# Kernel tuning notes

Measured on AMD Instinct MI355X. Metric: run time of the kernel, lower is better.

The kernel has to match this reference:

```python
import jax, jax.numpy as jnp
import numpy as np

NUM_HEADS = 16
HEAD_DIM = 64


def setup_inputs() -> dict:
    key = jax.random.key(0)
    k1, k2, k3 = jax.random.split(key, 3)
    B, S, D = 2, 2048, 1024
    scale = 1.0 / np.sqrt(D)
    return {
        "x": jax.random.normal(k1, (B, S, D), dtype=jnp.float32),
        "W_qkv": jax.random.normal(k2, (D, 3 * D), dtype=jnp.float32) * scale,
        "b_qkv": jnp.zeros((3 * D,), dtype=jnp.float32),
        "W_o": jax.random.normal(k3, (D, D), dtype=jnp.float32) * scale,
        "b_o": jnp.zeros((D,), dtype=jnp.float32),
    }


def reference(x, W_qkv, b_qkv, W_o, b_o):
    B, S, D = x.shape
    H, Hd = NUM_HEADS, HEAD_DIM
    qkv = x @ W_qkv + b_qkv                      # [B, S, 3D]
    qkv = qkv.reshape(B, S, H, 3 * Hd).transpose(0, 2, 1, 3)  # [B, H, S, 3Hd]
    q, k, v = jnp.split(qkv, 3, axis=-1)         # each [B, H, S, Hd]
    # negative squared Euclidean distance: -(|q|^2 - 2 q.k + |k|^2)
    q_sq = jnp.sum(q * q, axis=-1)[..., :, None]   # [B, H, S, 1]
    k_sq = jnp.sum(k * k, axis=-1)[..., None, :]   # [B, H, 1, S]
    qk = jnp.einsum("bhsd,bhtd->bhst", q, k)       # [B, H, S, S]
    logits = -(q_sq - 2.0 * qk + k_sq)
    attn = jax.nn.softmax(logits, axis=-1)
    vals = jnp.einsum("bhst,bhtd->bhsd", attn, v)  # [B, H, S, Hd]
    vals = vals.transpose(0, 2, 1, 3).reshape(B, S, D)
    return vals @ W_o + b_o
```

## Files before the change

kernel.cpp:

```cpp
#include <hip/hip_runtime.h>
#include <hip/hip_bf16.h>

#define NUM_B   2
#define SEQ     2048
#define DMODEL  1024
#define NH      16
#define HD      64
#define M_TOT   (NUM_B * SEQ)
#define N_QKV   (3 * DMODEL)
#define LOG2E   1.4426950408889634f
#define EXP_BIAS 96.0f

typedef __attribute__((ext_vector_type(8))) short short8v;
typedef __attribute__((ext_vector_type(4))) float float4v;
typedef unsigned short ushort_t;

__device__ __forceinline__ ushort_t f2bf(float x) {
    unsigned u = __builtin_bit_cast(unsigned, x);
    u = u + 0x7FFFu + ((u >> 16) & 1u);
    return (ushort_t)(u >> 16);
}
__device__ __forceinline__ float bf2f(ushort_t h) {
    unsigned u = ((unsigned)h) << 16;
    return __builtin_bit_cast(float, u);
}
__device__ __forceinline__ void gll16(const void* g, void* l) {
    __builtin_amdgcn_global_load_lds(
        (const __attribute__((address_space(1))) unsigned int*)g,
        (__attribute__((address_space(3))) unsigned int*)l, 16, 0, 0);
}
__device__ __forceinline__ int sw4(int r) { return (r & 3) ^ ((r >> 2) & 3); }

__global__ __launch_bounds__(256) void prep_kernel(
    const float* __restrict__ Wq, const float* __restrict__ Wo,
    const float* __restrict__ Xf,
    ushort_t* __restrict__ WqT_hi, ushort_t* __restrict__ WqT_lo,
    ushort_t* __restrict__ WoT,
    ushort_t* __restrict__ Xhi, ushort_t* __restrict__ Xlo)
{
    const int bid = blockIdx.x;
    const int t = threadIdx.x;

    if (bid >= 1024) {
        size_t base = (size_t)(bid - 1024) * 4096 + t * 16;
        float xs[16];
        *(float4v*)&xs[0]  = *(const float4v*)(Xf + base);
        *(float4v*)&xs[4]  = *(const float4v*)(Xf + base + 4);
        *(float4v*)&xs[8]  = *(const float4v*)(Xf + base + 8);
        *(float4v*)&xs[12] = *(const float4v*)(Xf + base + 12);
        short8v h0, h1, l0, l1;
        #pragma unroll
        for (int e = 0; e < 8; e++) {
            ushort_t a = f2bf(xs[e]), b = f2bf(xs[8 + e]);
            h0[e] = (short)a; h1[e] = (short)b;
            l0[e] = (short)f2bf(xs[e] - bf2f(a));
            l1[e] = (short)f2bf(xs[8 + e] - bf2f(b));
        }
        *(short8v*)(Xhi + base) = h0; *(short8v*)(Xhi + base + 8) = h1;
        *(short8v*)(Xlo + base) = l0; *(short8v*)(Xlo + base + 8) = l1;
        return;
    }

    __shared__ float Tf[64][65];
    const float* src; ushort_t *dhi, *dlo; int N, k0, n0;
    if (bid < 768) {
        int kt = bid / 48, nt = bid % 48;
        src = Wq; N = N_QKV; dhi = WqT_hi; dlo = WqT_lo;
        k0 = kt * 64; n0 = nt * 64;
    } else {
        int tid = bid - 768;
        int kt = tid >> 4, nt = tid & 15;
        src = Wo; N = DMODEL; dhi = WoT; dlo = nullptr;
        k0 = kt * 64; n0 = nt * 64;
    }
    {
        int r = t >> 2, c0 = (t & 3) * 16;
        const float* srow = src + (size_t)(k0 + r) * N + n0 + c0;
        #pragma unroll
        for (int u = 0; u < 4; u++) {
            float4v f = *(const float4v*)(srow + 4 * u);
            #pragma unroll
            for (int e = 0; e < 4; e++) Tf[r][c0 + 4 * u + e] = f[e];
        }
    }
    __syncthreads();
    {
        int nl = t >> 2, kc = (t & 3) * 16;
        short8v h0, h1, l0, l1;
        #pragma unroll
        for (int e = 0; e < 8; e++) {
            float x0 = Tf[kc + e][nl];
            float x1 = Tf[kc + 8 + e][nl];
            ushort_t a = f2bf(x0), b = f2bf(x1);
            h0[e] = (short)a; h1[e] = (short)b;
            l0[e] = (short)f2bf(x0 - bf2f(a));
            l1[e] = (short)f2bf(x1 - bf2f(b));
        }
        ushort_t* o = dhi + (size_t)(n0 + nl) * 1024 + k0 + kc;
        *(short8v*)o = h0; *(short8v*)(o + 8) = h1;
        if (dlo) {
            ushort_t* o2 = dlo + (size_t)(n0 + nl) * 1024 + k0 + kc;
            *(short8v*)o2 = l0; *(short8v*)(o2 + 8) = l1;
        }
    }
}

template<bool PRE>
__global__ __launch_bounds__(256) void qkv_mfma_kernel(
    const float* __restrict__ X,
    const ushort_t* __restrict__ Xhi, const ushort_t* __restrict__ Xlo,
    const ushort_t* __restrict__ WqT_hi, const ushort_t* __restrict__ WqT_lo,
    const float* __restrict__ bias,
    ushort_t* __restrict__ Qhi, ushort_t* __restrict__ Qlo,
    ushort_t* __restrict__ Khi, ushort_t* __restrict__ Klo,
    ushort_t* __restrict__ Vout,
    float* __restrict__ Qsq, float* __restrict__ Ksq)
{
    __shared__ ushort_t AS2[2 * 128 * 32];
    __shared__ ushort_t BS [2 * 128 * 32];
    const int LO = 128 * 32;
    const int t = threadIdx.x;
    const int w = t >> 6, lane = t & 63;
    const int quad = (t >> 4) & 3, ln = t & 15;
    const int wr = w >> 1, wc = w & 1;
    const int m0 = blockIdx.y * 128, n0 = blockIdx.x * 128;
    const int g = blockIdx.x * 2 + wc;
    const int h = g / 3, part = g % 3;

    const ushort_t* gA[2]; ushort_t* lA[2];
    const float* aptr = nullptr;
    ushort_t *ast_hi0, *ast_hi1, *ast_lo0, *ast_lo1;
    size_t xlo_off = 0;
    if constexpr (PRE) {
        #pragma unroll
        for (int i = 0; i < 2; i++) {
            int c = 256 * i + 64 * w + lane;
            int r = c >> 2, kbp = c & 3;
            gA[i] = Xhi + (size_t)(m0 + r) * 1024 + 8 * (kbp ^ sw4(r));
            lA[i] = &AS2[(256 * i + 64 * w) * 8];
        }
        xlo_off = (size_t)(Xlo - Xhi);
    } else {
        const int arow = t >> 1, akh = t & 1;
        aptr = X + (size_t)(m0 + arow) * DMODEL + 16 * akh;
        const int asw = sw4(arow);
        ast_hi0 = &AS2[arow * 32 + (((2 * akh) ^ asw) << 3)];
        ast_hi1 = &AS2[arow * 32 + (((2 * akh + 1) ^ asw) << 3)];
        ast_lo0 = &AS2[LO + arow * 32 + (((2 * akh) ^ asw) << 3)];
        ast_lo1 = &AS2[LO + arow * 32 + (((2 * akh + 1) ^ asw) << 3)];
    }

    const ushort_t* gB[2]; ushort_t* lB[2];
    #pragma unroll
    for (int i = 0; i < 2; i++) {
        int c = 256 * i + 64 * w + lane;
        int n = c >> 2, kbp = c & 3;
        gB[i] = WqT_hi + (size_t)(n0 + n) * 1024 + 8 * (kbp ^ sw4(n));
        lB[i] = &BS[(256 * i + 64 * w) * 8];
    }
    const size_t lo_goff = (size_t)(WqT_lo - WqT_hi);

    int aoff[4], boff[4];
    #pragma unroll
    for (int i = 0; i < 4; i++) {
        int m_l = 64 * wr + 16 * i + ln;
        aoff[i] = m_l * 32 + ((quad ^ sw4(m_l)) << 3);
        int n_l = 64 * wc + 16 * i + ln;
        boff[i] = n_l * 32 + ((quad ^ sw4(n_l)) << 3);
    }

    float4v acc[4][4];
    #pragma unroll
    for (int i = 0; i < 4; i++)
        #pragma unroll
        for (int j = 0; j < 4; j++) acc[i][j] = (float4v){0.f, 0.f, 0.f, 0.f};

    for (int k0 = 0; k0 < DMODEL; k0 += 32) {
        __syncthreads();
        #pragma unroll
        for (int i = 0; i < 2; i++) {
            gll16(gB[i] + k0, lB[i]);
            gll16(gB[i] + k0 + lo_goff, lB[i] + LO);
        }
        if constexpr (PRE) {
            #pragma unroll
            for (int i = 0; i < 2; i++) {
                gll16(gA[i] + k0, lA[i]);
                gll16(gA[i] + k0 + xlo_off, lA[i] + LO);
            }
        } else {
            float xs[16];
            *(float4v*)&xs[0]  = *(const float4v*)(aptr + k0);
            *(float4v*)&xs[4]  = *(const float4v*)(aptr + k0 + 4);
            *(float4v*)&xs[8]  = *(const float4v*)(aptr + k0 + 8);
            *(float4v*)&xs[12] = *(const float4v*)(aptr + k0 + 12);
            short8v h0, h1, l0, l1;
            #pragma unroll
            for (int e = 0; e < 8; e++) {
                ushort_t a = f2bf(xs[e]), b = f2bf(xs[8 + e]);
                h0[e] = (short)a; h1[e] = (short)b;
                l0[e] = (short)f2bf(xs[e] - bf2f(a));
                l1[e] = (short)f2bf(xs[8 + e] - bf2f(b));
            }
            *(short8v*)ast_hi0 = h0; *(short8v*)ast_hi1 = h1;
            *(short8v*)ast_lo0 = l0; *(short8v*)ast_lo1 = l1;
        }
        __syncthreads();

        short8v ah[4], al[4], bh[4], bl[4];
        #pragma unroll
        for (int i = 0; i < 4; i++) {
            ah[i] = *(short8v*)&AS2[aoff[i]];
            al[i] = *(short8v*)&AS2[LO + aoff[i]];
            bh[i] = *(short8v*)&BS[boff[i]];
            bl[i] = *(short8v*)&BS[LO + boff[i]];
        }
        if (part != 2) {
            #pragma unroll
            for (int mt = 0; mt < 4; mt++)
                #pragma unroll
                for (int nt = 0; nt < 4; nt++) {
                    acc[mt][nt] = __builtin_amdgcn_mfma_f32_16x16x32_bf16(ah[mt], bh[nt], acc[mt][nt], 0, 0, 0);
                    acc[mt][nt] = __builtin_amdgcn_mfma_f32_16x16x32_bf16(ah[mt], bl[nt], acc[mt][nt], 0, 0, 0);
                    acc[mt][nt] = __builtin_amdgcn_mfma_f32_16x16x32_bf16(al[mt], bh[nt], acc[mt][nt], 0, 0, 0);
                }
        } else {
            #pragma unroll
            for (int mt = 0; mt < 4; mt++)
                #pragma unroll
                for (int nt = 0; nt < 4; nt++)
                    acc[mt][nt] = __builtin_amdgcn_mfma_f32_16x16x32_bf16(ah[mt], bh[nt], acc[mt][nt], 0, 0, 0);
        }
    }

    float bvv[4];
    #pragma unroll
    for (int nt = 0; nt < 4; nt++) bvv[nt] = bias[64 * g + 16 * nt + ln];

    #pragma unroll
    for (int mt = 0; mt < 4; mt++) {
        #pragma unroll
        for (int r = 0; r < 4; r++) {
            int m = m0 + 64 * wr + 16 * mt + 4 * quad + r;
            int bb = m >> 11, s = m & (SEQ - 1);
            size_t hsrow = (size_t)(bb * NH + h) * SEQ + s;
            size_t rowbase = hsrow * HD;
            float vv[4];
            #pragma unroll
            for (int nt = 0; nt < 4; nt++) vv[nt] = acc[mt][nt][r] + bvv[nt];
            if (part == 0) {
                float sq = 0.f;
                #pragma unroll
                for (int nt = 0; nt < 4; nt++) {
                    float v = vv[nt];
                    sq += v * v;
                    float v2 = v * (2.0f * LOG2E);
                    ushort_t hb = f2bf(v2);
                    Qhi[rowbase + 16 * nt + ln] = hb;
                    Qlo[rowbase + 16 * nt + ln] = f2bf(v2 - bf2f(hb));
                }
                sq += __shfl_xor(sq, 1); sq += __shfl_xor(sq, 2);
                sq += __shfl_xor(sq, 4); sq += __shfl_xor(sq, 8);
                if (ln == 0) Qsq[hsrow] = sq * LOG2E - EXP_BIAS;
            } else if (part == 1) {
                float sq = 0.f;
                #pragma unroll
                for (int nt = 0; nt < 4; nt++) {
                    float v = vv[nt];
                    sq += v * v;
                    ushort_t hb = f2bf(v);
                    Khi[rowbase + 16 * nt + ln] = hb;
                    Klo[rowbase + 16 * nt + ln] = f2bf(v - bf2f(hb));
                }
                sq += __shfl_xor(sq, 1); sq += __shfl_xor(sq, 2);
                sq += __shfl_xor(sq, 4); sq += __shfl_xor(sq, 8);
                if (ln == 0) Ksq[hsrow] = sq * LOG2E;
            } else {
                if constexpr (PRE) {
                    #pragma unroll
                    for (int nt = 0; nt < 4; nt++)
                        Vout[((size_t)(bb * NH + h) * 64 + 16 * nt + ln) * SEQ + s] = f2bf(vv[nt]);
                } else {
                    #pragma unroll
                    for (int nt = 0; nt < 4; nt++)
                        Vout[rowbase + 16 * nt + ln] = f2bf(vv[nt]);
                }
            }
        }
    }
}

template<bool PRE>
__global__ __launch_bounds__(256, 4) void attn_mfma_kernel(
    const ushort_t* __restrict__ Qhi, const ushort_t* __restrict__ Qlo,
    const ushort_t* __restrict__ Khi, const ushort_t* __restrict__ Klo,
    const ushort_t* __restrict__ Vsrc,
    const float* __restrict__ Qsq, const float* __restrict__ Ksq,
    ushort_t* __restrict__ vals)
{
    __shared__ ushort_t KS[2 * 64 * 64];
    __shared__ ushort_t VtS [64 * 64];
    __shared__ ushort_t PsS [64 * 72];
    const int LO = 64 * 64;

    const int t    = threadIdx.x;
    const int w    = t >> 6, lane = t & 63;
    const int quad = (t >> 4) & 3, ln = t & 15;
    const int bh   = blockIdx.y;
    const int q0   = blockIdx.x * 64;
    const size_t base  = (size_t)bh * SEQ * HD;
    const size_t baseS = (size_t)bh * SEQ;

    short8v qhi[2], qlo[2];
    float4v qsq4;
    {
        size_t ro = base + (size_t)(q0 + 16 * w + ln) * HD + quad * 8;
        qhi[0] = *(const short8v*)(Qhi + ro);
        qhi[1] = *(const short8v*)(Qhi + ro + 32);
        qlo[0] = *(const short8v*)(Qlo + ro);
        qlo[1] = *(const short8v*)(Qlo + ro + 32);
        qsq4 = *(const float4v*)(Qsq + baseS + q0 + 16 * w + 4 * quad);
    }

    const ushort_t* gK[2]; ushort_t* lK[2];
    #pragma unroll
    for (int i = 0; i < 2; i++) {
        int c = 256 * i + 64 * w + lane;
        int key = c >> 3, dbp = c & 7;
        gK[i] = Khi + base + (size_t)key * HD + 8 * (dbp ^ (key & 7));
        lK[i] = &KS[(256 * i + 64 * w) * 8];
    }
    const size_t kloff = (size_t)(Klo - Khi);

    const ushort_t* gV[2]; ushort_t* lV[2];
    if constexpr (PRE) {
        #pragma unroll
        for (int i = 0; i < 2; i++) {
            int c = 256 * i + 64 * w + lane;
            int d = c >> 3, kc = c & 7;
            gV[i] = Vsrc + ((size_t)bh * 64 + d) * SEQ + 8 * (kc ^ (d & 7));
            lV[i] = &VtS[(256 * i + 64 * w) * 8];
        }
    }

    float4v accO[4];
    float lsum[4];
    #pragma unroll
    for (int nt = 0; nt < 4; nt++) accO[nt] = (float4v){0.f, 0.f, 0.f, 0.f};
    #pragma unroll
    for (int r = 0; r < 4; r++) lsum[r] = 0.f;

    for (int kt = 0; kt < SEQ; kt += 64) {
        __syncthreads();
        #pragma unroll
        for (int i = 0; i < 2; i++) {
            gll16(gK[i] + (size_t)kt * HD, lK[i]);
            gll16(gK[i] + (size_t)kt * HD + kloff, lK[i] + LO);
        }
        if constexpr (PRE) {
            #pragma unroll
            for (int i = 0; i < 2; i++)
                gll16(gV[i] + kt, lV[i]);
        } else {
            #pragma unroll
            for (int i = 0; i < 2; i++) {
                int c = t + 256 * i;
                int key = c >> 3, db = c & 7;
                short8v v8 = *(const short8v*)(Vsrc + base + (size_t)(kt + key) * HD + 8 * db);
                #pragma unroll
                for (int e = 0; e < 8; e++) {
                    int col = key ^ (e << 3);
                    VtS[(8 * db + e) * 64 + col] = (ushort_t)v8[e];
                }
            }
        }
        float ksq_c[4];
        #pragma unroll
        for (int nt = 0; nt < 4; nt++)
            ksq_c[nt] = Ksq[baseS + kt + 16 * nt + ln];
        __syncthreads();

        float4v accS[4];
        #pragma unroll
        for (int nt = 0; nt < 4; nt++) accS[nt] = (float4v){0.f, 0.f, 0.f, 0.f};

        #pragma unroll
        for (int nt = 0; nt < 4; nt++) {
            int keyrow = 16 * nt + ln;
            #pragma unroll
            for (int c = 0; c < 2; c++) {
                int db  = quad + 4 * c;
                int off = keyrow * 64 + ((db ^ (keyrow & 7)) << 3);
                short8v bh_ = *(short8v*)&KS[off];
                short8v bl_ = *(short8v*)&KS[LO + off];
                accS[nt] = __builtin_amdgcn_mfma_f32_16x16x32_bf16(qhi[c], bh_, accS[nt], 0, 0, 0);
                accS[nt] = __builtin_amdgcn_mfma_f32_16x16x32_bf16(qhi[c], bl_, accS[nt], 0, 0, 0);
                accS[nt] = __builtin_amdgcn_mfma_f32_16x16x32_bf16(qlo[c], bh_, accS[nt], 0, 0, 0);
            }
        }

        #pragma unroll
        for (int nt = 0; nt < 4; nt++) {
            float pv[4];
            #pragma unroll
            for (int r = 0; r < 4; r++) {
                float p = exp2f(accS[nt][r] - ksq_c[nt] - qsq4[r]);
                lsum[r] += p;
                pv[r] = p;
            }
            unsigned int pk01, pk23;
            asm("v_cvt_pk_bf16_f32 %0, %1, %2" : "=v"(pk01) : "v"(pv[0]), "v"(pv[1]));
            asm("v_cvt_pk_bf16_f32 %0, %1, %2" : "=v"(pk23) : "v"(pv[2]), "v"(pv[3]));
            ushort_t* pp = &PsS[(16 * w + 4 * quad) * 72 + 16 * nt + ln];
            pp[0]       = (ushort_t)(pk01 & 0xffffu);
            pp[72]      = (ushort_t)(pk01 >> 16);
            pp[144]     = (ushort_t)(pk23 & 0xffffu);
            pp[216]     = (ushort_t)(pk23 >> 16);
        }
        __syncthreads();

        #pragma unroll
        for (int c = 0; c < 2; c++) {
            short8v aP = *(short8v*)&PsS[(16 * w + ln) * 72 + quad * 8 + 32 * c];
            #pragma unroll
            for (int nt = 0; nt < 4; nt++) {
                int drow = 16 * nt + ln;
                int db   = quad + 4 * c;
                int off  = drow * 64 + ((db ^ (drow & 7)) << 3);
                short8v bV = *(short8v*)&VtS[off];
                accO[nt] = __builtin_amdgcn_mfma_f32_16x16x32_bf16(aP, bV, accO[nt], 0, 0, 0);
            }
        }
    }

    const int bb = bh >> 4, h = bh & 15;
    float inv[4];
    #pragma unroll
    for (int r = 0; r < 4; r++) {
        float s = lsum[r];
        s += __shfl_xor(s, 1); s += __shfl_xor(s, 2);
        s += __shfl_xor(s, 4); s += __shfl_xor(s, 8);
        inv[r] = 1.f / s;
    }
    #pragma unroll
    for (int nt = 0; nt < 4; nt++)
        #pragma unroll
        for (int r = 0; r < 4; r++) {
            int row = q0 + 16 * w + 4 * quad + r;
            vals[(size_t)(bb * SEQ + row) * DMODEL + h * 64 + 16 * nt + ln] =
                f2bf(accO[nt][r] * inv[r]);
        }
}

__global__ __launch_bounds__(256) void out_mfma_kernel(
    const ushort_t* __restrict__ Ab, const ushort_t* __restrict__ BT,
    const float* __restrict__ bias, float* __restrict__ out)
{
    __shared__ ushort_t AS[128 * 32], BSo[128 * 32];
    const int t = threadIdx.x;
    const int w = t >> 6, lane = t & 63;
    const int quad = (t >> 4) & 3, ln = t & 15;
    const int wr = w >> 1, wc = w & 1;
    const int m0 = blockIdx.y * 128, n0 = blockIdx.x * 128;

    const ushort_t* gA[2]; const ushort_t* gB[2];
    ushort_t *lA[2], *lB[2];
    #pragma unroll
    for (int i = 0; i < 2; i++) {
        int c = 256 * i + 64 * w + lane;
        int r = c >> 2, kbp = c & 3;
        gA[i] = Ab + (size_t)(m0 + r) * 1024 + 8 * (kbp ^ sw4(r));
        gB[i] = BT + (size_t)(n0 + r) * 1024 + 8 * (kbp ^ sw4(r));
        lA[i] = &AS[(256 * i + 64 * w) * 8];
        lB[i] = &BSo[(256 * i + 64 * w) * 8];
    }
    int aoff[4], boff[4];
    #pragma unroll
    for (int i = 0; i < 4; i++) {
        int m_l = 64 * wr + 16 * i + ln;
        aoff[i] = m_l * 32 + ((quad ^ sw4(m_l)) << 3);
        int n_l = 64 * wc + 16 * i + ln;
        boff[i] = n_l * 32 + ((quad ^ sw4(n_l)) << 3);
    }

    float4v acc[4][4];
    #pragma unroll
    for (int i = 0; i < 4; i++)
        #pragma unroll
        for (int j = 0; j < 4; j++) acc[i][j] = (float4v){0.f, 0.f, 0.f, 0.f};

    for (int k0 = 0; k0 < DMODEL; k0 += 32) {
        __syncthreads();
        #pragma unroll
        for (int i = 0; i < 2; i++) {
            gll16(gA[i] + k0, lA[i]);
            gll16(gB[i] + k0, lB[i]);
        }
        __syncthreads();
        short8v a[4], b[4];
        #pragma unroll
        for (int i = 0; i < 4; i++) {
            a[i] = *(short8v*)&AS[aoff[i]];
            b[i] = *(short8v*)&BSo[boff[i]];
        }
        #pragma unroll
        for (int mt = 0; mt < 4; mt++)
            #pragma unroll
            for (int nt = 0; nt < 4; nt++)
                acc[mt][nt] = __builtin_amdgcn_mfma_f32_16x16x32_bf16(a[mt], b[nt], acc[mt][nt], 0, 0, 0);
    }

    #pragma unroll
    for (int nt = 0; nt < 4; nt++) {
        int n = n0 + 64 * wc + 16 * nt + ln;
        float bv = bias[n];
        #pragma unroll
        for (int mt = 0; mt < 4; mt++)
            #pragma unroll
            for (int r = 0; r < 4; r++) {
                int m = m0 + 64 * wr + 16 * mt + 4 * quad + r;
                out[(size_t)m * DMODEL + n] = acc[mt][nt][r] + bv;
            }
    }
}

extern "C" void kernel_launch(void* const* d_in, const int* in_sizes, int n_in,
                              void* d_out, int out_size, void* d_ws, size_t ws_size,
                              hipStream_t stream) {
    const float* x     = (const float*)d_in[0];
    const float* W_qkv = (const float*)d_in[1];
    const float* b_qkv = (const float*)d_in[2];
    const float* W_o   = (const float*)d_in[3];
    const float* b_o   = (const float*)d_in[4];
    float* out = (float*)d_out;

    const size_t WQT = (size_t)N_QKV * DMODEL;
    const size_t WO  = (size_t)DMODEL * DMODEL;
    const size_t QE  = (size_t)NUM_B * NH * SEQ * HD;
    const size_t SQN = (size_t)NUM_B * NH * SEQ;

    const size_t NEED = (2 * WQT + WO + 5 * QE + 2 * QE) * 2 + 2 * SQN * 4;
    const bool pre = (ws_size >= NEED);

    ushort_t* ws     = (ushort_t*)d_ws;
    ushort_t* WqT_hi = ws;
    ushort_t* WqT_lo = WqT_hi + WQT;
    ushort_t* WoT    = WqT_lo + WQT;
    ushort_t* Qhi    = WoT + WO;
    ushort_t* Qlo    = Qhi + QE;
    ushort_t* Khi    = Qlo + QE;
    ushort_t* Klo    = Khi + QE;
    ushort_t* Vx     = Klo + QE;
    float*    Qsq; float* Ksq;
    ushort_t* valsb; ushort_t* Xhi = nullptr; ushort_t* Xlo = nullptr;

    if (pre) {
        Qsq   = (float*)(Vx + QE);
        Ksq   = Qsq + SQN;
        Xhi   = (ushort_t*)(Ksq + SQN);
        Xlo   = Xhi + QE;
        valsb = WqT_hi;
    } else {
        valsb = Vx + QE;
        Qsq   = (float*)(valsb + QE);
        Ksq   = Qsq + SQN;
    }

    prep_kernel<<<pre ? 2048 : 1024, 256, 0, stream>>>(
        W_qkv, W_o, x, WqT_hi, WqT_lo, WoT, Xhi, Xlo);
    if (pre) {
        qkv_mfma_kernel<true><<<dim3(N_QKV / 128, M_TOT / 128), 256, 0, stream>>>(
            x, Xhi, Xlo, WqT_hi, WqT_lo, b_qkv, Qhi, Qlo, Khi, Klo, Vx, Qsq, Ksq);
        attn_mfma_kernel<true><<<dim3(SEQ / 64, NUM_B * NH), 256, 0, stream>>>(
            Qhi, Qlo, Khi, Klo, Vx, Qsq, Ksq, valsb);
    } else {
        qkv_mfma_kernel<false><<<dim3(N_QKV / 128, M_TOT / 128), 256, 0, stream>>>(
            x, nullptr, nullptr, WqT_hi, WqT_lo, b_qkv, Qhi, Qlo, Khi, Klo, Vx, Qsq, Ksq);
        attn_mfma_kernel<false><<<dim3(SEQ / 64, NUM_B * NH), 256, 0, stream>>>(
            Qhi, Qlo, Khi, Klo, Vx, Qsq, Ksq, valsb);
    }
    out_mfma_kernel<<<dim3(DMODEL / 128, M_TOT / 128), 256, 0, stream>>>(
        valsb, WoT, b_o, out);
}
```

Measured before the change: 311.0 us.

## Add 256x256-tile QKV GEMM kernel with part-specialized split-bf16 precision

Adds a new QKV projection kernel that uses 512 threads and a 256x256 output tile, with double-buffered LDS staging via direct global-to-LDS loads. Each block handles a single Q, K or V part across four heads. The three-term hi/lo bf16 compensation is applied only to the Q/K parts, while V uses one bf16 MFMA. This aims to raise data reuse per LDS load and to cut MFMA and load work for V. In exchange it uses much more LDS and registers per block, which lowers occupancy.

```diff
diff --git a/kernel.cpp b/kernel.cpp
--- a/kernel.cpp
+++ b/kernel.cpp
@@ -101,6 +101,169 @@
         if (dlo) {
             ushort_t* o2 = dlo + (size_t)(n0 + nl) * 1024 + k0 + kc;
             *(short8v*)o2 = l0; *(short8v*)(o2 + 8) = l1;
+        }
+    }
+}
+
+__global__ __launch_bounds__(512, 2) void qkv_mfma256_kernel(
+    const ushort_t* __restrict__ Xhi, const ushort_t* __restrict__ Xlo,
+    const ushort_t* __restrict__ WqT_hi, const ushort_t* __restrict__ WqT_lo,
+    const float* __restrict__ bias,
+    ushort_t* __restrict__ Qhi, ushort_t* __restrict__ Qlo,
+    ushort_t* __restrict__ Khi, ushort_t* __restrict__ Klo,
+    ushort_t* __restrict__ Vout,
+    float* __restrict__ Qsq, float* __restrict__ Ksq)
+{
+    __shared__ ushort_t AS [2 * 2 * 8192];
+    __shared__ ushort_t BSh[2 * 2 * 8192];
+    const int SLAB = 8192;
+    const int BUFS = 2 * SLAB;
+
+    const int t    = threadIdx.x;
+    const int w    = t >> 6;
+    const int quad = (t >> 4) & 3, ln = t & 15;
+    const int wr = w >> 2, wc = w & 3;
+    const int bx = blockIdx.x, by = blockIdx.y;
+    const int p  = bx >> 2, bq = bx & 3;
+    const int m0 = by * 256;
+    const bool qk = (p != 2);
+    const int h  = 4 * bq + wc;
+    const int g  = p + 3 * h;
+
+    const ushort_t* gA[2]; const ushort_t* gB[2]; int lOff[2];
+    #pragma unroll
+    for (int i = 0; i < 2; i++) {
+        int c = 512 * i + t;
+        int r = c >> 2, kb = c & 3;
+        gA[i] = Xhi + (size_t)(m0 + r) * 1024 + 8 * (kb ^ sw4(r));
+        int hj = 4 * bq + (r >> 6);
+        int ng = 192 * hj + 64 * p + (r & 63);
+        gB[i] = WqT_hi + (size_t)ng * 1024 + 8 * (kb ^ sw4(r));
+        lOff[i] = (512 * i + 64 * w) * 8;
+    }
+    const size_t xlo_off = (size_t)(Xlo - Xhi);
+    const size_t wlo_off = (size_t)(WqT_lo - WqT_hi);
+
+    int aoff[8], boff[4];
+    #pragma unroll
+    for (int mt = 0; mt < 8; mt++) {
+        int m_l = 128 * wr + 16 * mt + ln;
+        aoff[mt] = m_l * 32 + ((quad ^ sw4(m_l)) << 3);
+    }
+    #pragma unroll
+    for (int nt = 0; nt < 4; nt++) {
+        int n_l = 64 * wc + 16 * nt + ln;
+        boff[nt] = n_l * 32 + ((quad ^ sw4(n_l)) << 3);
+    }
+
+    float4v acc[8][4];
+    #pragma unroll
+    for (int i = 0; i < 8; i++)
+        #pragma unroll
+        for (int j = 0; j < 4; j++) acc[i][j] = (float4v){0.f, 0.f, 0.f, 0.f};
+
+    auto stage = [&](int ks, int buf) {
+        const int kk = 32 * ks;
+        ushort_t* Ab = &AS [buf * BUFS];
+        ushort_t* Bb = &BSh[buf * BUFS];
+        #pragma unroll
+        for (int i = 0; i < 2; i++) {
+            gll16(gA[i] + kk, Ab + lOff[i]);
+            gll16(gB[i] + kk, Bb + lOff[i]);
+        }
+        if (qk) {
+            #pragma unroll
+            for (int i = 0; i < 2; i++) {
+                gll16(gA[i] + kk + xlo_off, Ab + SLAB + lOff[i]);
+                gll16(gB[i] + kk + wlo_off, Bb + SLAB + lOff[i]);
+            }
+        }
+    };
+
+    const int NKS = DMODEL / 32;
+    stage(0, 0);
+    __syncthreads();
+
+    for (int ks = 0; ks < NKS; ks++) {
+        const int buf = ks & 1;
+        if (ks + 1 < NKS) stage(ks + 1, buf ^ 1);
+
+        const ushort_t* Ab = &AS [buf * BUFS];
+        const ushort_t* Bb = &BSh[buf * BUFS];
+
+        short8v bh4[4], bl4[4];
+        #pragma unroll
+        for (int nt = 0; nt < 4; nt++) {
+            bh4[nt] = *(const short8v*)(Bb + boff[nt]);
+            if (qk) bl4[nt] = *(const short8v*)(Bb + SLAB + boff[nt]);
+        }
+        #pragma unroll
+        for (int mt = 0; mt < 8; mt++) {
+            short8v ahm = *(const short8v*)(Ab + aoff[mt]);
+            if (qk) {
+                short8v alm = *(const short8v*)(Ab + SLAB + aoff[mt]);
+                #pragma unroll
+                for (int nt = 0; nt < 4; nt++) {
+                    acc[mt][nt] = __builtin_amdgcn_mfma_f32_16x16x32_bf16(ahm, bh4[nt], acc[mt][nt], 0, 0, 0);
+                    acc[mt][nt] = __builtin_amdgcn_mfma_f32_16x16x32_bf16(ahm, bl4[nt], acc[mt][nt], 0, 0, 0);
+                    acc[mt][nt] = __builtin_amdgcn_mfma_f32_16x16x32_bf16(alm, bh4[nt], acc[mt][nt], 0, 0, 0);
+                }
+            } else {
+                #pragma unroll
+                for (int nt = 0; nt < 4; nt++)
+                    acc[mt][nt] = __builtin_amdgcn_mfma_f32_16x16x32_bf16(ahm, bh4[nt], acc[mt][nt], 0, 0, 0);
+            }
+        }
+        __syncthreads();
+    }
+
+    float bvv[4];
+    #pragma unroll
+    for (int nt = 0; nt < 4; nt++) bvv[nt] = bias[64 * g + 16 * nt + ln];
+
+    #pragma unroll
+    for (int mt = 0; mt < 8; mt++) {
+        #pragma unroll
+        for (int r = 0; r < 4; r++) {
+            int m = m0 + 128 * wr + 16 * mt + 4 * quad + r;
+            int bb = m >> 11, s = m & (SEQ - 1);
+            size_t hsrow = (size_t)(bb * NH + h) * SEQ + s;
+            size_t rowbase = hsrow * HD;
+            float vv[4];
+            #pragma unroll
+            for (int nt = 0; nt < 4; nt++) vv[nt] = acc[mt][nt][r] + bvv[nt];
+            if (p == 0) {
+                float sq = 0.f;
+                #pragma unroll
+                for (int nt = 0; nt < 4; nt++) {
+                    float v = vv[nt];
+                    sq += v * v;
+                    float v2 = v * (2.0f * LOG2E);
+                    ushort_t hb = f2bf(v2);
+                    Qhi[rowbase + 16 * nt + ln] = hb;
+                    Qlo[rowbase + 16 * nt + ln] = f2bf(v2 - bf2f(hb));
+                }
+                sq += __shfl_xor(sq, 1); sq += __shfl_xor(sq, 2);
+                sq += __shfl_xor(sq, 4); sq += __shfl_xor(sq, 8);
+                if (ln == 0) Qsq[hsrow] = sq * LOG2E - EXP_BIAS;
+            } else if (p == 1) {
+                float sq = 0.f;
+                #pragma unroll
+                for (int nt = 0; nt < 4; nt++) {
+                    float v = vv[nt];
+                    sq += v * v;
+                    ushort_t hb = f2bf(v);
+                    Khi[rowbase + 16 * nt + ln] = hb;
+                    Klo[rowbase + 16 * nt + ln] = f2bf(v - bf2f(hb));
+                }
+                sq += __shfl_xor(sq, 1); sq += __shfl_xor(sq, 2);
+                sq += __shfl_xor(sq, 4); sq += __shfl_xor(sq, 8);
+                if (ln == 0) Ksq[hsrow] = sq * LOG2E;
+            } else {
+                #pragma unroll
+                for (int nt = 0; nt < 4; nt++)
+                    Vout[((size_t)(bb * NH + h) * 64 + 16 * nt + ln) * SEQ + s] = f2bf(vv[nt]);
+            }
         }
     }
 }
@@ -276,15 +439,9 @@
                 sq += __shfl_xor(sq, 4); sq += __shfl_xor(sq, 8);
                 if (ln == 0) Ksq[hsrow] = sq * LOG2E;
             } else {
-                if constexpr (PRE) {
-                    #pragma unroll
-                    for (int nt = 0; nt < 4; nt++)
-                        Vout[((size_t)(bb * NH + h) * 64 + 16 * nt + ln) * SEQ + s] = f2bf(vv[nt]);
-                } else {
-                    #pragma unroll
-                    for (int nt = 0; nt < 4; nt++)
-                        Vout[rowbase + 16 * nt + ln] = f2bf(vv[nt]);
-                }
+                #pragma unroll
+                for (int nt = 0; nt < 4; nt++)
+                    Vout[rowbase + 16 * nt + ln] = f2bf(vv[nt]);
             }
         }
     }
@@ -569,8 +726,8 @@
     prep_kernel<<<pre ? 2048 : 1024, 256, 0, stream>>>(
         W_qkv, W_o, x, WqT_hi, WqT_lo, WoT, Xhi, Xlo);
     if (pre) {
-        qkv_mfma_kernel<true><<<dim3(N_QKV / 128, M_TOT / 128), 256, 0, stream>>>(
-            x, Xhi, Xlo, WqT_hi, WqT_lo, b_qkv, Qhi, Qlo, Khi, Klo, Vx, Qsq, Ksq);
+        qkv_mfma256_kernel<<<dim3(12, M_TOT / 256), 512, 0, stream>>>(
+            Xhi, Xlo, WqT_hi, WqT_lo, b_qkv, Qhi, Qlo, Khi, Klo, Vx, Qsq, Ksq);
         attn_mfma_kernel<true><<<dim3(SEQ / 64, NUM_B * NH), 256, 0, stream>>>(
             Qhi, Qlo, Khi, Klo, Vx, Qsq, Ksq, valsb);
     } else {
```

Result: faster. 297.8 us (-4.2%).
